# Performance work log

Hardware: AMD Instinct MI355X
Metric: run time of the kernel (lower is better)

Reference implementation:

```python
import jax, jax.numpy as jnp
import numpy as np

N = 768          # number of atoms
DIM = 3
F = 128          # feature width
N_RBF = 32       # gaussian radial basis size
CUTOFF = 5.0
NUM_CHAINS = 4
T_IN_K = 300.0
TTIME = 20.0
KB = 8.617330337217213e-05   # Boltzmann constant, eV/K (ASE units.kB)
BOX = 24.8                   # box side so that ~26 neighbors/atom within cutoff
GAMMA = 1.0 / (CUTOFF / N_RBF) ** 2  # RBF width


def setup_inputs() -> dict:
    key = jax.random.key(0)
    ks = jax.random.split(key, 12)
    q = jax.random.uniform(ks[0], (N, DIM), dtype=jnp.float32) * BOX
    v = jax.random.normal(ks[1], (N, DIM), dtype=jnp.float32) * 0.01
    p_eta = jax.random.normal(ks[2], (NUM_CHAINS,), dtype=jnp.float32) * 0.1
    mass = jax.random.uniform(ks[3], (N,), dtype=jnp.float32, minval=1.0, maxval=20.0)
    atomic_numbers = jax.random.randint(ks[4], (N,), 0, 100, dtype=jnp.int32)
    embed = jax.random.normal(ks[5], (100, F), dtype=jnp.float32) * 0.1
    W1 = jax.random.normal(ks[6], (N_RBF, F), dtype=jnp.float32) / np.sqrt(N_RBF)
    b1 = jnp.zeros((F,), dtype=jnp.float32)
    W2 = jax.random.normal(ks[7], (F, F), dtype=jnp.float32) / np.sqrt(F)
    b2 = jnp.zeros((F,), dtype=jnp.float32)
    W3 = jax.random.normal(ks[8], (F, F), dtype=jnp.float32) / np.sqrt(F)
    w_out = jax.random.normal(ks[9], (F,), dtype=jnp.float32) / np.sqrt(F)
    return dict(v=v, q=q, p_eta=p_eta, mass=mass, embed=embed, W1=W1, b1=b1,
                W2=W2, b2=b2, W3=W3, w_out=w_out, atomic_numbers=atomic_numbers)


def _energy(q, atomic_numbers, embed, W1, b1, W2, b2, W3, w_out):
    """SchNet-style cutoff-graph potential energy (scalar)."""
    h = embed[atomic_numbers]                                   # [N,F]
    disp = q[:, None, :] - q[None, :, :]                        # [N,N,3]
    d2 = jnp.sum(disp * disp, axis=-1)                          # [N,N]
    eye = jnp.eye(N, dtype=bool)
    mask = (d2 < CUTOFF ** 2) & (~eye)                          # cutoff neighbor list (dense mask)
    d = jnp.sqrt(jnp.where(mask, d2, 1.0))                      # safe sqrt off-graph
    centers = jnp.linspace(0.0, CUTOFF, N_RBF, dtype=q.dtype)
    rbf = jnp.exp(-GAMMA * (d[..., None] - centers) ** 2)       # [N,N,n_rbf]
    filt = jax.nn.relu(rbf @ W1 + b1) @ W2 + b2                 # [N,N,F]
    filt = jnp.where(mask[..., None], filt, 0.0)
    m = jnp.einsum('ijf,jf->if', filt, h)                       # message aggregation
    h = h + jax.nn.relu(m @ W3)
    return jnp.sum(h @ w_out)


def reference(v, q, p_eta, mass, embed, W1, b1, W2, b2, W3, w_out, atomic_numbers):
    kT = T_IN_K * KB
    n_dof = N * DIM
    target_ke = 0.5 * n_dof * kT
    Q = 2.0 * jnp.array([n_dof * kT * TTIME ** 2] + [kT * TTIME ** 2] * (NUM_CHAINS - 1),
                        dtype=v.dtype)
    p = v * mass[:, None]                                       # momenta
    current_ke = 0.5 * jnp.sum(p * p / mass[:, None])
    # f = -dE/dq (torch: -results['energy_grad'])
    f = -jax.grad(_energy)(q, atomic_numbers, embed, W1, b1, W2, b2, W3, w_out)
    coupled_forces = (p_eta[0] * p.reshape(-1) / Q[0]).reshape(-1, 3)
    dvdt = (f - coupled_forces) / mass[:, None]
    dpeta_first = 2.0 * (current_ke - target_ke) - p_eta[0] * p_eta[1] / Q[1]
    dpeta_mid = p_eta[:-2] ** 2 / Q[:-2] - kT - p_eta[1:-1] * p_eta[2:] / Q[2:]
    dpeta_last = p_eta[-2] ** 2 / Q[-2] - kT
    dpeta_dt = jnp.concatenate([dpeta_first[None], dpeta_mid, dpeta_last[None]])
    return (dvdt, v, dpeta_dt)
```

## Files before the change

kernel.cpp:

```cpp
#include <hip/hip_runtime.h>
#include <math.h>

#define N_ATOMS 768
#define FD 128
#define NRBF 32
#define MAXN 64
#define PPF 32
#define NTHREADS 512
#define TST 136
#define RSTU 40

constexpr float  CUT2   = 25.0f;
constexpr float  GAMMA_ = 40.96f;
constexpr float  CSTEP  = 5.0f / 31.0f;
constexpr double KB_D   = 8.617330337217213e-05;
constexpr double KT_D   = 300.0 * KB_D;
constexpr float  KT_F   = (float)KT_D;
constexpr float  TARGET_KE = (float)(0.5 * 2304.0 * KT_D);
constexpr float  Q0_F   = (float)(2.0 * 2304.0 * KT_D * 400.0);
constexpr float  QI_F   = (float)(2.0 * KT_D * 400.0);

#define DVDT_OFF 0
#define V_OFF    (3 * N_ATOMS)
#define PETA_OFF (6 * N_ATOMS)

using short8v = __attribute__((ext_vector_type(8))) short;
using f32x4   = __attribute__((ext_vector_type(4))) float;

#define MFMA_B16 __builtin_amdgcn_mfma_f32_16x16x32_bf16

__device__ __forceinline__ unsigned short f2bf(float x) {
    unsigned int u = __float_as_uint(x);
    u += 0x7FFF + ((u >> 16) & 1);
    return (unsigned short)(u >> 16);
}
__device__ __forceinline__ float bf2f(unsigned short h) {
    return __uint_as_float(((unsigned int)h) << 16);
}


__global__ __launch_bounds__(256) void prep_kernel(
    const int* __restrict__ z, const float* __restrict__ embed,
    const float* __restrict__ W1, const float* __restrict__ W2,
    const float* __restrict__ W3,
    float* __restrict__ h, float* __restrict__ W3T,
    unsigned short* __restrict__ w1fh, unsigned short* __restrict__ w1fl,
    unsigned short* __restrict__ w2fh, unsigned short* __restrict__ w2fl,
    unsigned short* __restrict__ w2bh, unsigned short* __restrict__ w2bl,
    float* __restrict__ f_acc)
{
    int g = blockIdx.x * 256 + threadIdx.x;
    if (g < N_ATOMS * FD) h[g] = embed[z[g >> 7] * FD + (g & 127)];
    if (g < FD * FD) {
        int r = g >> 7, c = g & 127;
        float w = W2[g];
        unsigned short hb = f2bf(w);
        unsigned short lb = f2bf(w - bf2f(hb));
        w2bh[g] = hb;
        w2bl[g] = lb;
        w2fh[c * FD + r] = hb;
        w2fl[c * FD + r] = lb;
        W3T[c * FD + r] = W3[g];
        if (g < NRBF * FD) {
            float w1v = W1[g];
            unsigned short h1 = f2bf(w1v);
            w1fh[c * NRBF + r] = h1;
            w1fl[c * NRBF + r] = f2bf(w1v - bf2f(h1));
        }
    }
    if (g < 3 * N_ATOMS) f_acc[g] = 0.f;
}

__global__ __launch_bounds__(NTHREADS) void atom_kernel(
    const float* __restrict__ q,
    const unsigned short* __restrict__ w1fh, const unsigned short* __restrict__ w1fl,
    const float* __restrict__ b1,
    const unsigned short* __restrict__ w2fh, const unsigned short* __restrict__ w2fl,
    const unsigned short* __restrict__ w2bh, const unsigned short* __restrict__ w2bl,
    const float* __restrict__ b2, const float* __restrict__ h,
    const float* __restrict__ W3, const float* __restrict__ W3T,
    const float* __restrict__ wout,
    float* __restrict__ f_acc)
{
    __shared__ int   nj[MAXN];
    __shared__ float nd[MAXN], ndx[MAXN], ndy[MAXN], ndz[MAXN];
    __shared__ int   cnt_s;
    __shared__ __align__(16) unsigned short rbf_h[PPF * RSTU];
    __shared__ __align__(16) unsigned short rbf_l[PPF * RSTU];
    __shared__ __align__(16) unsigned short a1h[PPF * TST];
    __shared__ __align__(16) unsigned short a1l[PPF * TST];
    __shared__ __align__(16) unsigned short crbf_h[PPF * RSTU];
    __shared__ __align__(16) unsigned short crbf_l[PPF * RSTU];
    __shared__ __align__(16) unsigned short ts_h[PPF * TST];
    __shared__ __align__(16) unsigned short ts_l[PPF * TST];
    __shared__ float mrow[FD], gb[FD], mbrow[FD];
    __shared__ float part[NTHREADS];
    __shared__ float sred[8 * PPF];

    int i = blockIdx.x, t = threadIdx.x;
    if (t == 0) cnt_s = 0;
    __syncthreads();
    float qx = q[i*3], qy = q[i*3+1], qz = q[i*3+2];
    for (int j = t; j < N_ATOMS; j += NTHREADS) {
        if (j == i) continue;
        float dx = qx - q[j*3], dy = qy - q[j*3+1], dz = qz - q[j*3+2];
        float d2 = dx*dx + dy*dy + dz*dz;
        if (d2 < CUT2) {
            int p = atomicAdd(&cnt_s, 1);
            if (p < MAXN) { nj[p] = j; nd[p] = sqrtf(d2);
                            ndx[p] = dx; ndy[p] = dy; ndz[p] = dz; }
        }
    }
    __syncthreads();
    int cnt = min(cnt_s, MAXN);
    if (cnt == 0) return;

    int wid = t >> 6, lane = t & 63;
    int lr = lane & 15, lg = lane >> 4;
    int c0 = wid * 16 + lr;
    float bb0 = b1[c0];
    float b2c0 = b2[c0];
    float macc0 = 0.f;
    unsigned int mk0 = 0, mk1 = 0;

    auto fwd_pass = [&](int p0, unsigned int& mk_out) {
#pragma unroll
        for (int e = 0; e < 2; e++) {
            int idx = t + e * NTHREADS;
            int p = idx >> 5, k = idx & 31;
            int pp = p0 + p;
            float d = (pp < cnt) ? nd[pp] : 1.0f;
            float u = d - CSTEP * (float)k;
            float r = __expf(-GAMMA_ * u * u);
            unsigned short hb = f2bf(r);
            rbf_h[p * RSTU + k] = hb;
            rbf_l[p * RSTU + k] = f2bf(r - bf2f(hb));
        }
        __syncthreads();

        float h00[4], h10[4];
#pragma unroll
        for (int r = 0; r < 4; r++) {
            int pA = p0 + lg * 4 + r, pB = pA + 16;
            bool vA = pA < cnt, vB = pB < cnt;
            int jA = vA ? nj[pA] : 0, jB = vB ? nj[pB] : 0;
            h00[r] = vA ? h[jA * FD + c0] : 0.f;
            h10[r] = vB ? h[jB * FD + c0] : 0.f;
        }

        {
            f32x4 u00 = {bb0,bb0,bb0,bb0};
            f32x4 u10 = {bb0,bb0,bb0,bb0};
            short8v rh0 = *(const short8v*)(rbf_h + lr * RSTU + lg * 8);
            short8v rh1 = *(const short8v*)(rbf_h + (16+lr) * RSTU + lg * 8);
            short8v rl0 = *(const short8v*)(rbf_l + lr * RSTU + lg * 8);
            short8v rl1 = *(const short8v*)(rbf_l + (16+lr) * RSTU + lg * 8);
            short8v bh0 = *(const short8v*)(w1fh + c0 * NRBF + lg * 8);
            short8v bl0 = *(const short8v*)(w1fl + c0 * NRBF + lg * 8);
            u00 = MFMA_B16(rh0, bh0, u00, 0,0,0);
            u10 = MFMA_B16(rh1, bh0, u10, 0,0,0);
            u00 = MFMA_B16(rh0, bl0, u00, 0,0,0);
            u10 = MFMA_B16(rh1, bl0, u10, 0,0,0);
            u00 = MFMA_B16(rl0, bh0, u00, 0,0,0);
            u10 = MFMA_B16(rl1, bh0, u10, 0,0,0);
            unsigned int mk = 0;
#pragma unroll
            for (int r = 0; r < 4; r++) {
                int pA = lg * 4 + r, pB = 16 + lg * 4 + r;
                float v; unsigned short hb;
                if (u00[r] > 0.f) mk |= 1u << r;
                if (u10[r] > 0.f) mk |= 1u << (4 + r);
                v = fmaxf(u00[r], 0.f); hb = f2bf(v);
                a1h[pA * TST + c0] = hb; a1l[pA * TST + c0] = f2bf(v - bf2f(hb));
                v = fmaxf(u10[r], 0.f); hb = f2bf(v);
                a1h[pB * TST + c0] = hb; a1l[pB * TST + c0] = f2bf(v - bf2f(hb));
            }
            mk_out = mk;
        }
        __syncthreads();

        {
            f32x4 acc00 = {0.f,0.f,0.f,0.f};
            f32x4 acc10 = {0.f,0.f,0.f,0.f};
#pragma unroll
            for (int ks = 0; ks < 4; ks++) {
                int kb = ks * 32 + lg * 8;
                short8v ah0 = *(const short8v*)(a1h + (lr     ) * TST + kb);
                short8v ah1 = *(const short8v*)(a1h + (16 + lr) * TST + kb);
                short8v al0 = *(const short8v*)(a1l + (lr     ) * TST + kb);
                short8v al1 = *(const short8v*)(a1l + (16 + lr) * TST + kb);
                short8v bh0 = *(const short8v*)(w2fh + c0 * FD + kb);
                short8v bl0 = *(const short8v*)(w2fl + c0 * FD + kb);
                acc00 = MFMA_B16(ah0, bh0, acc00, 0,0,0);
                acc10 = MFMA_B16(ah1, bh0, acc10, 0,0,0);
                acc00 = MFMA_B16(ah0, bl0, acc00, 0,0,0);
                acc10 = MFMA_B16(ah1, bl0, acc10, 0,0,0);
                acc00 = MFMA_B16(al0, bh0, acc00, 0,0,0);
                acc10 = MFMA_B16(al1, bh0, acc10, 0,0,0);
            }
#pragma unroll
            for (int r = 0; r < 4; r++) {
                macc0 += (acc00[r] + b2c0) * h00[r] + (acc10[r] + b2c0) * h10[r];
            }
        }
        __syncthreads();
    };

    fwd_pass(0, mk0);
    if (cnt > PPF) fwd_pass(PPF, mk1);

    {
        float r0 = macc0 + __shfl_xor(macc0, 16, 64);
        r0 += __shfl_xor(r0, 32, 64);
        if (lg == 0) mrow[c0] = r0;
    }
    __syncthreads();

    {
        int c = t & 127, hh = t >> 7;
        int f0h = hh * 32;
        float g = 0.f;
#pragma unroll 4
        for (int f4 = f0h; f4 < f0h + 32; f4 += 4) {
            float4 w  = *(const float4*)(W3T + c * FD + f4);
            float4 mr = *(const float4*)(mrow + f4);
            g += mr.x*w.x + mr.y*w.y + mr.z*w.z + mr.w*w.w;
        }
        part[t] = g;
        __syncthreads();
        if (t < FD)
            gb[t] = (part[t] + part[t + 128] + part[t + 256] + part[t + 384] > 0.f)
                    ? wout[t] : 0.f;
        __syncthreads();
        float mb = 0.f;
#pragma unroll 4
        for (int f4 = f0h; f4 < f0h + 32; f4 += 4) {
            float4 w  = *(const float4*)(W3 + c * FD + f4);
            float4 gv = *(const float4*)(gb + f4);
            mb += gv.x*w.x + gv.y*w.y + gv.z*w.z + gv.w*w.w;
        }
        part[t] = mb;
        __syncthreads();
        if (t < FD) mbrow[t] = part[t] + part[t + 128] + part[t + 256] + part[t + 384];
    }
    __syncthreads();

    float iax = 0.f, iay = 0.f, iaz = 0.f;

    auto bwd_pass = [&](int p0, unsigned int mk) {
#pragma unroll
        for (int e = 0; e < 2; e++) {
            int idx = t + e * NTHREADS;
            int p = idx >> 5, k = idx & 31;
            int pp = p0 + p;
            float d = (pp < cnt) ? nd[pp] : 1.0f;
            float u = d - CSTEP * (float)k;
            float r = __expf(-GAMMA_ * u * u);
            float cd = -2.f * GAMMA_ * u * r;
            unsigned short hc = f2bf(cd);
            crbf_h[p * RSTU + k] = hc;
            crbf_l[p * RSTU + k] = f2bf(cd - bf2f(hc));
        }
#pragma unroll
        for (int e = 0; e < 2; e++) {
            int idx = t + e * NTHREADS;
            int p = idx >> 5, c4g = (idx & 31) * 4;
            int pp = p0 + p;
            ushort4 hv = {0,0,0,0}, lv = {0,0,0,0};
            if (pp < cnt) {
                float4 mb4 = *(const float4*)(mbrow + c4g);
                float4 hj4 = *(const float4*)(h + nj[pp] * FD + c4g);
                float v0 = mb4.x*hj4.x, v1 = mb4.y*hj4.y;
                float v2 = mb4.z*hj4.z, v3 = mb4.w*hj4.w;
                hv.x = f2bf(v0); lv.x = f2bf(v0 - bf2f(hv.x));
                hv.y = f2bf(v1); lv.y = f2bf(v1 - bf2f(hv.y));
                hv.z = f2bf(v2); lv.z = f2bf(v2 - bf2f(hv.z));
                hv.w = f2bf(v3); lv.w = f2bf(v3 - bf2f(hv.w));
            }
            *(ushort4*)(ts_h + p * TST + c4g) = hv;
            *(ushort4*)(ts_l + p * TST + c4g) = lv;
        }
        __syncthreads();

        f32x4 e00 = {0.f,0.f,0.f,0.f};
        f32x4 e10 = {0.f,0.f,0.f,0.f};
        {
            short8v ch0 = *(const short8v*)(crbf_h + lr * RSTU + lg * 8);
            short8v ch1 = *(const short8v*)(crbf_h + (16+lr) * RSTU + lg * 8);
            short8v cl0 = *(const short8v*)(crbf_l + lr * RSTU + lg * 8);
            short8v cl1 = *(const short8v*)(crbf_l + (16+lr) * RSTU + lg * 8);
            short8v bh0 = *(const short8v*)(w1fh + c0 * NRBF + lg * 8);
            short8v bl0 = *(const short8v*)(w1fl + c0 * NRBF + lg * 8);
            e00 = MFMA_B16(ch0, bh0, e00, 0,0,0);
            e10 = MFMA_B16(ch1, bh0, e10, 0,0,0);
            e00 = MFMA_B16(ch0, bl0, e00, 0,0,0);
            e10 = MFMA_B16(ch1, bl0, e10, 0,0,0);
            e00 = MFMA_B16(cl0, bh0, e00, 0,0,0);
            e10 = MFMA_B16(cl1, bh0, e10, 0,0,0);
        }
#pragma unroll
        for (int r = 0; r < 4; r++) {
            e00[r] = (mk & (1u <<  r      )) ? e00[r] : 0.f;
            e10[r] = (mk & (1u << (4 + r))) ? e10[r] : 0.f;
        }

        f32x4 acc00 = {0.f,0.f,0.f,0.f};
        f32x4 acc10 = {0.f,0.f,0.f,0.f};
#pragma unroll
        for (int ks = 0; ks < 4; ks++) {
            int kb = ks * 32 + lg * 8;
            short8v ah0 = *(const short8v*)(ts_h + (lr     ) * TST + kb);
            short8v ah1 = *(const short8v*)(ts_h + (16 + lr) * TST + kb);
            short8v al0 = *(const short8v*)(ts_l + (lr     ) * TST + kb);
            short8v al1 = *(const short8v*)(ts_l + (16 + lr) * TST + kb);
            short8v bh0 = *(const short8v*)(w2bh + c0 * FD + kb);
            short8v bl0 = *(const short8v*)(w2bl + c0 * FD + kb);
            acc00 = MFMA_B16(ah0, bh0, acc00, 0,0,0);
            acc10 = MFMA_B16(ah1, bh0, acc10, 0,0,0);
            acc00 = MFMA_B16(ah0, bl0, acc00, 0,0,0);
            acc10 = MFMA_B16(ah1, bl0, acc10, 0,0,0);
            acc00 = MFMA_B16(al0, bh0, acc00, 0,0,0);
            acc10 = MFMA_B16(al1, bh0, acc10, 0,0,0);
        }

        float part8[8];
#pragma unroll
        for (int r = 0; r < 4; r++) {
            part8[r]     = acc00[r] * e00[r];
            part8[4 + r] = acc10[r] * e10[r];
        }
#pragma unroll
        for (int mask = 1; mask < 16; mask <<= 1) {
#pragma unroll
            for (int e = 0; e < 8; e++) part8[e] += __shfl_xor(part8[e], mask, 64);
        }
        if (lr == 0) {
#pragma unroll
            for (int r = 0; r < 4; r++) {
                sred[wid * PPF + lg * 4 + r]      = part8[r];
                sred[wid * PPF + 16 + lg * 4 + r] = part8[4 + r];
            }
        }
        __syncthreads();

        if (t < PPF && p0 + t < cnt) {
            float s = 0.f;
#pragma unroll
            for (int w = 0; w < 8; w++) s += sred[w * PPF + t];
            int pp = p0 + t;
            float coef = s / nd[pp];
            float fx = coef * ndx[pp];
            float fy = coef * ndy[pp];
            float fz = coef * ndz[pp];
            iax += fx; iay += fy; iaz += fz;
            atomicAdd(f_acc + nj[pp]*3 + 0, fx);
            atomicAdd(f_acc + nj[pp]*3 + 1, fy);
            atomicAdd(f_acc + nj[pp]*3 + 2, fz);
        }
        __syncthreads();
    };

    bwd_pass(0, mk0);
    if (cnt > PPF) bwd_pass(PPF, mk1);

    if (t < PPF) {
#pragma unroll
        for (int mask = 1; mask < 32; mask <<= 1) {
            iax += __shfl_xor(iax, mask, 64);
            iay += __shfl_xor(iay, mask, 64);
            iaz += __shfl_xor(iaz, mask, 64);
        }
        if (t == 0) {
            atomicAdd(f_acc + i*3 + 0, -iax);
            atomicAdd(f_acc + i*3 + 1, -iay);
            atomicAdd(f_acc + i*3 + 2, -iaz);
        }
    }
}

__global__ __launch_bounds__(256) void fin_kernel(
    const float* __restrict__ v, const float* __restrict__ mass,
    const float* __restrict__ p_eta, const float* __restrict__ f_acc,
    float* __restrict__ out)
{
    __shared__ float red[256];
    int t = threadIdx.x;
    float ke = 0.f;
    float c = p_eta[0] / Q0_F;
    for (int idx = t; idx < 3 * N_ATOMS; idx += 256) {
        int a = idx / 3;
        float vv = v[idx], mi = mass[a];
        out[DVDT_OFF + idx] = (f_acc[idx] - c * vv * mi) / mi;
        out[V_OFF + idx] = vv;
        ke += 0.5f * mi * vv * vv;
    }
    red[t] = ke;
    __syncthreads();
    for (int s = 128; s > 0; s >>= 1) {
        if (t < s) red[t] += red[t + s];
        __syncthreads();
    }
    if (t == 0) {
        float k0 = red[0];
        float e0 = p_eta[0], e1 = p_eta[1], e2 = p_eta[2], e3 = p_eta[3];
        out[PETA_OFF + 0] = 2.f * (k0 - TARGET_KE) - e0 * e1 / QI_F;
        out[PETA_OFF + 1] = e0 * e0 / Q0_F - KT_F - e1 * e2 / QI_F;
        out[PETA_OFF + 2] = e1 * e1 / QI_F - KT_F - e2 * e3 / QI_F;
        out[PETA_OFF + 3] = e2 * e2 / QI_F - KT_F;
    }
}

extern "C" void kernel_launch(void* const* d_in, const int* in_sizes, int n_in,
                              void* d_out, int out_size, void* d_ws, size_t ws_size,
                              hipStream_t stream)
{
    const float* v     = (const float*)d_in[0];
    const float* q     = (const float*)d_in[1];
    const float* p_eta = (const float*)d_in[2];
    const float* mass  = (const float*)d_in[3];
    const float* embed = (const float*)d_in[4];
    const float* W1    = (const float*)d_in[5];
    const float* b1    = (const float*)d_in[6];
    const float* W2    = (const float*)d_in[7];
    const float* b2    = (const float*)d_in[8];
    const float* W3    = (const float*)d_in[9];
    const float* wout  = (const float*)d_in[10];
    const int*   z     = (const int*)d_in[11];
    float* out = (float*)d_out;

    float* h     = (float*)d_ws;
    float* W3T   = h + N_ATOMS * FD;
    float* f_acc = W3T + FD * FD;
    unsigned short* w2bh = (unsigned short*)(f_acc + 3 * N_ATOMS);
    unsigned short* w2bl = w2bh + FD * FD;
    unsigned short* w2fh = w2bl + FD * FD;
    unsigned short* w2fl = w2fh + FD * FD;
    unsigned short* w1fh = w2fl + FD * FD;
    unsigned short* w1fl = w1fh + NRBF * FD;

    prep_kernel<<<384, 256, 0, stream>>>(z, embed, W1, W2, W3, h, W3T,
                                         w1fh, w1fl, w2fh, w2fl, w2bh, w2bl,
                                         f_acc);
    atom_kernel<<<N_ATOMS, NTHREADS, 0, stream>>>(q, w1fh, w1fl, b1, w2fh, w2fl,
                                                  w2bh, w2bl, b2, h, W3, W3T, wout,
                                                  f_acc);
    fin_kernel<<<1, 256, 0, stream>>>(v, mass, p_eta, f_acc, out);
}
```

Measured before the change: 131.1 us.

## Alias forward/backward LDS buffers, prefetch neighbor features, and cut block barriers

The forward and backward staging buffers now share two LDS pools, shrinking the shared-memory footprint so more blocks can be resident per CU. The W3/W3T matvec reductions switch from an LDS partial-sum array with extra barriers to wave shuffles across the 16-lane groups. Neighbor feature rows for the first pass are loaded into registers early so that global-load latency overlaps the forward pass. Trailing barriers in each pass are moved so they run only when a second pass exists. The price is more live registers and a reliance on barrier placement being correct when buffers are aliased.

Result: faster. 128.5 us (-2.0%).

```diff
diff --git a/kernel.cpp b/kernel.cpp
--- a/kernel.cpp
+++ b/kernel.cpp
@@ -85,17 +85,19 @@
     __shared__ int   nj[MAXN];
     __shared__ float nd[MAXN], ndx[MAXN], ndy[MAXN], ndz[MAXN];
     __shared__ int   cnt_s;
-    __shared__ __align__(16) unsigned short rbf_h[PPF * RSTU];
-    __shared__ __align__(16) unsigned short rbf_l[PPF * RSTU];
-    __shared__ __align__(16) unsigned short a1h[PPF * TST];
-    __shared__ __align__(16) unsigned short a1l[PPF * TST];
-    __shared__ __align__(16) unsigned short crbf_h[PPF * RSTU];
-    __shared__ __align__(16) unsigned short crbf_l[PPF * RSTU];
-    __shared__ __align__(16) unsigned short ts_h[PPF * TST];
-    __shared__ __align__(16) unsigned short ts_l[PPF * TST];
+    __shared__ __align__(16) unsigned short poolR[2 * PPF * RSTU];
+    __shared__ __align__(16) unsigned short poolA[2 * PPF * TST];
     __shared__ float mrow[FD], gb[FD], mbrow[FD];
-    __shared__ float part[NTHREADS];
     __shared__ float sred[8 * PPF];
+
+    unsigned short* rbf_h  = poolR;
+    unsigned short* rbf_l  = poolR + PPF * RSTU;
+    unsigned short* crbf_h = poolR;
+    unsigned short* crbf_l = poolR + PPF * RSTU;
+    unsigned short* a1h  = poolA;
+    unsigned short* a1l  = poolA + PPF * TST;
+    unsigned short* ts_h = poolA;
+    unsigned short* ts_l = poolA + PPF * TST;
 
     int i = blockIdx.x, t = threadIdx.x;
     if (t == 0) cnt_s = 0;
@@ -122,6 +124,15 @@
     float b2c0 = b2[c0];
     float macc0 = 0.f;
     unsigned int mk0 = 0, mk1 = 0;
+
+    float4 hj0[2];
+#pragma unroll
+    for (int e = 0; e < 2; e++) {
+        int idx = t + e * NTHREADS;
+        int p = idx >> 5, c4g = (idx & 31) * 4;
+        hj0[e] = (p < cnt) ? *(const float4*)(h + nj[p] * FD + c4g)
+                           : make_float4(0.f, 0.f, 0.f, 0.f);
+    }
 
     auto fwd_pass = [&](int p0, unsigned int& mk_out) {
 #pragma unroll
@@ -203,11 +214,10 @@
                 macc0 += (acc00[r] + b2c0) * h00[r] + (acc10[r] + b2c0) * h10[r];
             }
         }
-        __syncthreads();
     };
 
     fwd_pass(0, mk0);
-    if (cnt > PPF) fwd_pass(PPF, mk1);
+    if (cnt > PPF) { __syncthreads(); fwd_pass(PPF, mk1); }
 
     {
         float r0 = macc0 + __shfl_xor(macc0, 16, 64);
@@ -217,37 +227,37 @@
     __syncthreads();
 
     {
-        int c = t & 127, hh = t >> 7;
-        int f0h = hh * 32;
+        int f0h = lg * 32;
         float g = 0.f;
-#pragma unroll 4
-        for (int f4 = f0h; f4 < f0h + 32; f4 += 4) {
-            float4 w  = *(const float4*)(W3T + c * FD + f4);
-            float4 mr = *(const float4*)(mrow + f4);
+#pragma unroll
+        for (int f4 = 0; f4 < 32; f4 += 4) {
+            float4 w  = *(const float4*)(W3T + c0 * FD + f0h + f4);
+            float4 mr = *(const float4*)(mrow + f0h + f4);
             g += mr.x*w.x + mr.y*w.y + mr.z*w.z + mr.w*w.w;
         }
-        part[t] = g;
-        __syncthreads();
-        if (t < FD)
-            gb[t] = (part[t] + part[t + 128] + part[t + 256] + part[t + 384] > 0.f)
-                    ? wout[t] : 0.f;
-        __syncthreads();
+        g += __shfl_xor(g, 16, 64);
+        g += __shfl_xor(g, 32, 64);
+        if (lg == 0) gb[c0] = (g > 0.f) ? wout[c0] : 0.f;
+    }
+    __syncthreads();
+    {
+        int f0h = lg * 32;
         float mb = 0.f;
-#pragma unroll 4
-        for (int f4 = f0h; f4 < f0h + 32; f4 += 4) {
-            float4 w  = *(const float4*)(W3 + c * FD + f4);
-            float4 gv = *(const float4*)(gb + f4);
+#pragma unroll
+        for (int f4 = 0; f4 < 32; f4 += 4) {
+            float4 w  = *(const float4*)(W3 + c0 * FD + f0h + f4);
+            float4 gv = *(const float4*)(gb + f0h + f4);
             mb += gv.x*w.x + gv.y*w.y + gv.z*w.z + gv.w*w.w;
         }
-        part[t] = mb;
-        __syncthreads();
-        if (t < FD) mbrow[t] = part[t] + part[t + 128] + part[t + 256] + part[t + 384];
+        mb += __shfl_xor(mb, 16, 64);
+        mb += __shfl_xor(mb, 32, 64);
+        if (lg == 0) mbrow[c0] = mb;
     }
     __syncthreads();
 
     float iax = 0.f, iay = 0.f, iaz = 0.f;
 
-    auto bwd_pass = [&](int p0, unsigned int mk) {
+    auto bwd_pass = [&](int p0, unsigned int mk, bool first) {
 #pragma unroll
         for (int e = 0; e < 2; e++) {
             int idx = t + e * NTHREADS;
@@ -269,7 +279,8 @@
             ushort4 hv = {0,0,0,0}, lv = {0,0,0,0};
             if (pp < cnt) {
                 float4 mb4 = *(const float4*)(mbrow + c4g);
-                float4 hj4 = *(const float4*)(h + nj[pp] * FD + c4g);
+                float4 hj4 = first ? hj0[e]
+                                   : *(const float4*)(h + nj[pp] * FD + c4g);
                 float v0 = mb4.x*hj4.x, v1 = mb4.y*hj4.y;
                 float v2 = mb4.z*hj4.z, v3 = mb4.w*hj4.w;
                 hv.x = f2bf(v0); lv.x = f2bf(v0 - bf2f(hv.x));
@@ -357,11 +368,10 @@
             atomicAdd(f_acc + nj[pp]*3 + 1, fy);
             atomicAdd(f_acc + nj[pp]*3 + 2, fz);
         }
-        __syncthreads();
     };
 
-    bwd_pass(0, mk0);
-    if (cnt > PPF) bwd_pass(PPF, mk1);
+    bwd_pass(0, mk0, true);
+    if (cnt > PPF) { __syncthreads(); bwd_pass(PPF, mk1, false); }
 
     if (t < PPF) {
 #pragma unroll
```
